# Kernel optimization log

Measured on AMD Instinct MI355X. Metric: run time of the kernel, lower is better.

## Reference

```python
import jax, jax.numpy as jnp
import numpy as np

H = 512       # hidden_dim == node_init_dim
N_MAX = 128   # max nodes (upper bound on ADD_NODE count)
L = 1024      # action sequence length (padded with -1)
NEG = -1e9    # mask value for invalid destination logits


def _gru(x, h, wih, whh, bih, bhh):
    # PyTorch nn.GRUCell math; gates packed as [r, z, n] along dim 0.
    gi = wih @ x + bih
    gh = whh @ h + bhh
    d = h.shape[0]
    r = jax.nn.sigmoid(gi[:d] + gh[:d])
    z = jax.nn.sigmoid(gi[d:2 * d] + gh[d:2 * d])
    n = jnp.tanh(gi[2 * d:] + r * gh[2 * d:])
    return (1.0 - z) * n + z * h


def _make_actions(rng):
    # Synthesize a grammatically valid DGMG teacher-forcing trace:
    # ADD_NODE=0, ADD_EDGE=1, CHOOSE_DEST=2, STOP_EDGE=3, STOP_NODE=4, pad=-1
    acts, ags = [], []
    cur = -1
    while len(acts) < L - 8 and cur < N_MAX - 1:
        acts.append(0); ags.append(0)
        cur += 1
        if cur > 0:
            for _ in range(int(rng.integers(1, 4))):
                if len(acts) >= L - 4:
                    break
                acts.append(1); ags.append(0)
                acts.append(2); ags.append(int(rng.integers(0, cur)))
            acts.append(3); ags.append(0)
    acts.append(4); ags.append(0)
    pad = L - len(acts)
    acts += [-1] * pad
    ags += [0] * pad
    return np.array(acts, np.int64), np.array(ags, np.int64)


def setup_inputs() -> dict:
    rng = np.random.default_rng(0)
    acts, ags = _make_actions(rng)
    key = jax.random.key(0)
    ks = jax.random.split(key, 12)
    s = 0.02
    p = lambda k, shape: jax.random.normal(k, shape, jnp.float32) * s
    return {
        "actions": jnp.asarray(acts),
        "args_seq": jnp.asarray(ags),
        "node_init": p(ks[0], (H,)),
        "w_nip": p(ks[1], (H, H)), "b_nip": jnp.zeros((H,), jnp.float32),
        "w_e1": p(ks[2], (H, 2 * H)), "b_e1": jnp.zeros((H,), jnp.float32),
        "w_e2": p(ks[3], (2, H)), "b_e2": jnp.zeros((2,), jnp.float32),
        "w_q": p(ks[4], (H, 2 * H)), "b_q": jnp.zeros((H,), jnp.float32),
        "w_k": p(ks[5], (H, H)), "b_k": jnp.zeros((H,), jnp.float32),
        "wih_n": p(ks[6], (3 * H, H)), "whh_n": p(ks[7], (3 * H, H)),
        "bih_n": jnp.zeros((3 * H,), jnp.float32), "bhh_n": jnp.zeros((3 * H,), jnp.float32),
        "wih_g": p(ks[8], (3 * H, H)), "whh_g": p(ks[9], (3 * H, H)),
        "bih_g": jnp.zeros((3 * H,), jnp.float32), "bhh_g": jnp.zeros((3 * H,), jnp.float32),
        "graph0": jnp.zeros((H,), jnp.float32),
    }


def reference(actions, args_seq, node_init, w_nip, b_nip, w_e1, b_e1, w_e2, b_e2,
              w_q, b_q, w_k, b_k, wih_n, whh_n, bih_n, bhh_n,
              wih_g, whh_g, bih_g, bhh_g, graph0):
    h0 = w_nip @ node_init + b_nip  # same fresh-node embedding for every ADD_NODE
    idx_range = jnp.arange(N_MAX)

    def edge_logits(g, curv):
        h = jax.nn.relu(w_e1 @ jnp.concatenate([g, curv]) + b_e1)
        return w_e2 @ h + b_e2  # (2,)

    def add_node(carry, arg):
        g, ne, cur, nll = carry
        cur2 = cur + 1
        ne2 = ne.at[cur2].set(h0)
        g2 = _gru(h0, g, wih_g, whh_g, bih_g, bhh_g)
        return (g2, ne2, cur2, nll)

    def add_edge(carry, arg):
        g, ne, cur, nll = carry
        nll2 = nll - jax.nn.log_softmax(edge_logits(g, ne[cur]))[0]
        return (g, ne, cur, nll2)

    def choose_dest(carry, arg):
        g, ne, cur, nll = carry
        curv = ne[cur]
        q = w_q @ jnp.concatenate([g, curv]) + b_q           # (H,)
        k = ne @ w_k.T + b_k                                  # (N_MAX, H)
        logits = jnp.where(idx_range < cur, k @ q, NEG)       # mask nodes >= cur
        nll2 = nll - jax.nn.log_softmax(logits)[arg]
        chosen = ne[arg]
        new_cur = _gru(chosen, curv, wih_n, whh_n, bih_n, bhh_n)
        ne2 = ne.at[cur].set(new_cur)
        g2 = _gru(new_cur, g, wih_g, whh_g, bih_g, bhh_g)
        return (g2, ne2, cur, nll2)

    def stop_edge(carry, arg):
        g, ne, cur, nll = carry
        nll2 = nll - jax.nn.log_softmax(edge_logits(g, ne[cur]))[1]
        return (g, ne, cur, nll2)

    def noop(carry, arg):
        return carry

    branches = [add_node, add_edge, choose_dest, stop_edge, noop]

    def step(carry, inp):
        a, arg = inp
        idx = jnp.where((a < 0) | (a >= 4), 4, a).astype(jnp.int32)
        return jax.lax.switch(idx, branches, carry, arg), None

    init = (graph0, jnp.zeros((N_MAX, H), graph0.dtype),
            jnp.int32(-1), jnp.zeros((), graph0.dtype))
    (g, ne, cur, nll), _ = jax.lax.scan(
        step, init, (actions.astype(jnp.int32), args_seq.astype(jnp.int32)))
    return nll
```

## Files before the change

kernel.cpp:

```cpp
#include <hip/hip_runtime.h>
#include <math.h>

#define NBLK 64
#define NTHR 576
#define LSEQ 1024

typedef unsigned int u32;
typedef unsigned short u16;
typedef unsigned long long u64;

__device__ __forceinline__ float bf2f(u16 u){ union{u32 i;float f;}v; v.i=(u32)u<<16; return v.f; }
__device__ __forceinline__ u16 f2bf(float f){ union{float f;u32 i;}v; v.f=f; u32 x=v.i;
  return (u16)((x + 0x7fffu + ((x>>16)&1u)) >> 16); }
__device__ __forceinline__ float u2f(u32 u){ union{u32 i;float f;}v; v.i=u; return v.f; }
__device__ __forceinline__ u32  f2u(float f){ union{float f;u32 i;}v; v.f=f; return v.i; }
__device__ __forceinline__ float sigm(float x){ return 1.f/(1.f+__expf(-x)); }

__device__ __forceinline__ u64 gld64(const u64* p){ return __hip_atomic_load(const_cast<u64*>(p), __ATOMIC_RELAXED, __HIP_MEMORY_SCOPE_AGENT); }
__device__ __forceinline__ void gst64(u64* p, u64 v){ __hip_atomic_store(p, v, __ATOMIC_RELAXED, __HIP_MEMORY_SCOPE_AGENT); }
__device__ __forceinline__ u64 pollt(const u64* p, u32 tag){
  u64 v; int n = 0;
  do { v = gld64(p); } while ((u32)(v>>32) != tag && ++n < (1<<20));
  return v;
}

__device__ __forceinline__ float wred(float a){
  a += __int_as_float(__builtin_amdgcn_update_dpp(0, __float_as_int(a), 0x111, 0xf, 0xf, true));
  a += __int_as_float(__builtin_amdgcn_update_dpp(0, __float_as_int(a), 0x112, 0xf, 0xf, true));
  a += __int_as_float(__builtin_amdgcn_update_dpp(0, __float_as_int(a), 0x114, 0xf, 0xf, true));
  a += __int_as_float(__builtin_amdgcn_update_dpp(0, __float_as_int(a), 0x118, 0xf, 0xf, true));
  a += __int_as_float(__builtin_amdgcn_update_dpp(0, __float_as_int(a), 0x142, 0xa, 0xf, true));
  a += __int_as_float(__builtin_amdgcn_update_dpp(0, __float_as_int(a), 0x143, 0xc, 0xf, true));
  return __int_as_float(__builtin_amdgcn_readlane(__float_as_int(a), 63));
}
__device__ __forceinline__ float wredsh(float a){
  #pragma unroll
  for (int off = 32; off; off >>= 1) a += __shfl_xor(a, off);
  return a;
}
__device__ __forceinline__ float wredmaxsh(float a){
  #pragma unroll
  for (int off = 32; off; off >>= 1) a = fmaxf(a, __shfl_xor(a, off));
  return a;
}

__device__ __forceinline__ float dot8p(uint4 w, float4 a, float4 b2){
  float s;
  s  = u2f(w.x<<16)*a.x  + u2f(w.x&0xffff0000u)*a.y;
  s += u2f(w.y<<16)*a.z  + u2f(w.y&0xffff0000u)*a.w;
  s += u2f(w.z<<16)*b2.x + u2f(w.z&0xffff0000u)*b2.y;
  s += u2f(w.w<<16)*b2.z + u2f(w.w&0xffff0000u)*b2.w;
  return s;
}
__device__ __forceinline__ float dot4f(float4 w, float4 x){
  return w.x*x.x + w.y*x.y + w.z*x.z + w.w*x.w;
}
__device__ __forceinline__ uint4 pk8(float4 a, float4 b2){
  uint4 r;
  r.x = (u32)f2bf(a.x)  | ((u32)f2bf(a.y)<<16);
  r.y = (u32)f2bf(a.z)  | ((u32)f2bf(a.w)<<16);
  r.z = (u32)f2bf(b2.x) | ((u32)f2bf(b2.y)<<16);
  r.w = (u32)f2bf(b2.z) | ((u32)f2bf(b2.w)<<16);
  return r;
}

#define SMEM_BYTES 150048

#define RUN_JOBS() do { \
  if (wv == 8){ \
    if (dBV && b == dBo1){ \
      u64 v_ = pollt(XS + dBSlot*64 + lane, dBTag); \
      float x0 = sA0 + bf2f((u16)(v_ & 0xffff)); \
      float x1 = sA1 + bf2f((u16)((v_>>16) & 0xffff)); \
      x0 = (lane < dBcur) ? x0 : -__builtin_inff(); \
      x1 = (lane + 64 < dBcur) ? x1 : -__builtin_inff(); \
      float m_ = wredmaxsh(fmaxf(x0, x1)); \
      float s_ = wredsh(__expf(x0 - m_) + __expf(x1 - m_)); \
      float la_ = (dBarg < 64) ? __shfl(x0, dBarg) : __shfl(x1, dBarg - 64); \
      if (lane == 0) nllw += (m_ + logf(s_)) - la_; \
    } \
    if (dAV && (b == dAo1 || b == dAo2)){ \
      const u64* P_ = XP + ((size_t)(dASlot*64 + lane))*64 + ((b == dAo2) ? 32 : 0); \
      float h0_ = 0.f, h1_ = 0.f; \
      for (int c_ = 0; c_ < 2; ++c_){ \
        u64 vv_[16]; int bad_; int nn_ = 0; \
        do { bad_ = 0; \
          _Pragma("unroll") for (int j_ = 0; j_ < 16; ++j_) vv_[j_] = gld64(P_ + c_*16 + j_); \
          _Pragma("unroll") for (int j_ = 0; j_ < 16; ++j_) bad_ |= ((u32)(vv_[j_]>>32) != dATag); \
        } while (bad_ && ++nn_ < (1<<20)); \
        _Pragma("unroll") for (int j_ = 0; j_ < 16; ++j_){ \
          h0_ += bf2f((u16)(vv_[j_] & 0xffff)); h1_ += bf2f((u16)((vv_[j_]>>16) & 0xffff)); } \
      } \
      if (b == dAo2) gst64(XS + dASlot*64 + lane, ((u64)dATag<<32) | (u32)f2bf(h0_) | ((u32)f2bf(h1_)<<16)); \
      else { sA0 = h0_; sA1 = h1_; } \
    } \
    if (aeV && b == aeOwn){ \
      u64 v_ = pollt(XE + aeSlot*64 + lane, aeTag); \
      float p0_ = wredsh(bf2f((u16)(v_ & 0xffff))); \
      float p1_ = wredsh(bf2f((u16)((v_>>16) & 0xffff))); \
      if (lane == 0){ \
        float l0_ = p0_ + be2_0, l1_ = p1_ + be2_1; \
        float m_ = fmaxf(l0_, l1_); \
        nllw += m_ + logf(__expf(l0_-m_) + __expf(l1_-m_)) - (aeSel ? l1_ : l0_); \
      } \
    } \
  } \
} while(0)

#define SHIFT_JOBS() do { \
  dBV = dAV; dBSlot = dASlot; dBo1 = dAo1; dBTag = dATag; dBcur = dAcur; dBarg = dAarg; \
  dAV = 0; aeV = 0; \
} while(0)

__global__ void __launch_bounds__(NTHR, 1)
dgmg_kernel(const int* __restrict__ actions, const int* __restrict__ argseq,
            const float* __restrict__ node_init, const float* __restrict__ w_nip, const float* __restrict__ b_nip,
            const float* __restrict__ w_e1, const float* __restrict__ b_e1,
            const float* __restrict__ w_e2, const float* __restrict__ b_e2,
            const float* __restrict__ w_q, const float* __restrict__ b_q,
            const float* __restrict__ w_k,
            const float* __restrict__ wih_n, const float* __restrict__ whh_n,
            const float* __restrict__ bih_n, const float* __restrict__ bhh_n,
            const float* __restrict__ wih_g, const float* __restrict__ whh_g,
            const float* __restrict__ bih_g, const float* __restrict__ bhh_g,
            const float* __restrict__ graph0,
            float* __restrict__ out, unsigned char* __restrict__ ws)
{
  extern __shared__ unsigned char smem[];
  u16* s_wihg = (u16*)smem;
  u16* s_whhg = s_wihg + 24*512;
  u16* s_wihn = s_whhg + 24*512;
  u16* s_whhn = s_wihn + 24*512;
  u16* s_we1  = s_whhn + 24*512;
  u16* s_wq   = s_we1 + 8*1024;
  float* s_g    = (float*)(s_wq + 8*1024);
  float* s_nc   = s_g + 512;
  float* s_curv = s_nc + 512;
  float* s_h0   = s_curv + 512;
  float* s_kloc = s_h0 + 512;
  float* s_bihg = s_kloc + 1024;
  float* s_bhhg = s_bihg + 24;
  float* s_bihn = s_bhhg + 24;
  float* s_bhhn = s_bihn + 24;
  float* s_be1  = s_bhhn + 24;
  float* s_bq   = s_be1 + 8;
  float* s_q8   = s_bq + 8;
  float* s_red  = s_q8 + 8;
  u16*   s_gin  = (u16*)(s_red + 16);

  const int b = blockIdx.x, tid = threadIdx.x;
  const int wv = tid >> 6, lane = tid & 63;
  const int d = b*8 + ((wv < 8) ? wv : 0);

  u64* Xng = (u64*)ws;
  u64* Xh  = Xng + 2048;
  u64* XE  = Xh + 512;
  u64* XP  = XE + 256;
  u64* XS  = XP + 16384;
  u64* XN  = XS + 256;

  if (tid < 24){
    int ld = tid/3, gt = tid%3;
    int row = gt*512 + b*8 + ld;
    s_bihg[tid] = bih_g[row]; s_bhhg[tid] = bhh_g[row];
    s_bihn[tid] = bih_n[row]; s_bhhn[tid] = bhh_n[row];
  }
  if (tid < 8){ s_be1[tid] = b_e1[b*8+tid]; s_bq[tid] = b_q[b*8+tid]; }

  for (int r = wv; r < 24; r += 9){
    int ld = r/3, gt = r%3;
    long grow = (long)(gt*512 + b*8 + ld) * 512;
    float4 a0, a1;
    a0 = *(const float4*)&wih_g[grow + lane*8]; a1 = *(const float4*)&wih_g[grow + lane*8 + 4];
    *(uint4*)&s_wihg[r*512 + lane*8] = pk8(a0, a1);
    a0 = *(const float4*)&whh_g[grow + lane*8]; a1 = *(const float4*)&whh_g[grow + lane*8 + 4];
    *(uint4*)&s_whhg[r*512 + lane*8] = pk8(a0, a1);
    a0 = *(const float4*)&wih_n[grow + lane*8]; a1 = *(const float4*)&wih_n[grow + lane*8 + 4];
    *(uint4*)&s_wihn[r*512 + lane*8] = pk8(a0, a1);
    a0 = *(const float4*)&whh_n[grow + lane*8]; a1 = *(const float4*)&whh_n[grow + lane*8 + 4];
    *(uint4*)&s_whhn[r*512 + lane*8] = pk8(a0, a1);
  }
  if (wv < 8){
    long grow = (long)(b*8 + wv) * 1024;
    #pragma unroll
    for (int h = 0; h < 2; ++h){
      float4 a0 = *(const float4*)&w_e1[grow + h*512 + lane*8];
      float4 a1 = *(const float4*)&w_e1[grow + h*512 + lane*8 + 4];
      *(uint4*)&s_we1[wv*1024 + h*512 + lane*8] = pk8(a0, a1);
      float4 q0 = *(const float4*)&w_q[grow + h*512 + lane*8];
      float4 q1 = *(const float4*)&w_q[grow + h*512 + lane*8 + 4];
      *(uint4*)&s_wq[wv*1024 + h*512 + lane*8] = pk8(q0, q1);
    }
  }
  float we2_0 = w_e2[d], we2_1 = w_e2[512+d];
  float be2_0 = b_e2[0], be2_1 = b_e2[1];
  float nllw = 0.f, sA0 = 0.f, sA1 = 0.f;

  int aeV=0, aeSlot=0, aeSel=0, aeOwn=0; u32 aeTag=0;
  int dAV=0, dASlot=0, dAo1=0, dAo2=0, dAcur=0, dAarg=0; u32 dATag=0;
  int dBV=0, dBSlot=0, dBo1=0, dBcur=0, dBarg=0; u32 dBTag=0;
  int ecnt=0, dcnt=0;

  if (tid < 512) s_g[tid] = node_init[tid];
  __syncthreads();
  float cbg_r=0,cbg_z=0,bg_ni=0,bg_nh=0, bh_gr=0,bh_gz=0;
  float bn_r=0,bn_z=0,bn_nh=0, fb_r=0,fb_z=0,fb_n=0, be1w=0,bqw=0;
  if (wv < 8){
    cbg_r = s_bihg[wv*3+0]+s_bhhg[wv*3+0];
    cbg_z = s_bihg[wv*3+1]+s_bhhg[wv*3+1];
    bg_ni = s_bihg[wv*3+2]; bg_nh = s_bhhg[wv*3+2];
    bh_gr = s_bhhg[wv*3+0]; bh_gz = s_bhhg[wv*3+1];
    bn_r = s_bhhn[wv*3+0]; bn_z = s_bhhn[wv*3+1]; bn_nh = s_bhhn[wv*3+2];
    fb_r = s_bihn[wv*3+0]; fb_z = s_bihn[wv*3+1]; fb_n = s_bihn[wv*3+2];
    be1w = s_be1[wv]; bqw = s_bq[wv];
    const float* wr = w_nip + (long)d*512;
    float4 wa = *(const float4*)&wr[lane*8], wb2 = *(const float4*)&wr[lane*8+4];
    float4 xa = *(float4*)&s_g[lane*8], xb = *(float4*)&s_g[lane*8+4];
    float h0d = wred(dot4f(wa,xa)+dot4f(wb2,xb)) + b_nip[d];
    if (lane == 0) gst64(&Xh[d], (1ull<<32) | f2u(h0d));
  }
  u32 ph = 2;

  float gi0r=0,gi0z=0,gi0n=0, ghn0r=0,ghn0z=0,ghn0n=0;
  int cur = -1, have_se = 0;
  bool first_an = true;

  for (int t = 0; t < LSEQ; ++t){
    int a = actions[t];
    if (a == 1) continue;
    if (a == 3){ have_se = 1; continue; }
    if (a < 0 || a >= 4) continue;

    int t1 = (t+1 < LSEQ) ? actions[t+1] : -1;
    int nxt = (t1 == 1);
    int i2 = (t+2 < LSEQ) ? t+2 : LSEQ-1;
    int chn = nxt ? argseq[i2] : 0;

    if (a == 0){
      int eslot = ecnt & 3;
      u32 tg = ph-1; int par = tg & 1;
      if (first_an){
        if (tid < 512){ u64 v = pollt(&Xh[tid], 1u); s_h0[tid] = u2f((u32)v); s_g[tid] = graph0[tid]; }
      } else {
        if (tid < 512){ u64 v = pollt(&Xng[(par*512+tid)*2+1], tg); s_g[tid] = u2f((u32)v); }
      }
      __syncthreads();
      RUN_JOBS();
      if (wv < 8){
        float4 xg_a = *(float4*)&s_g[lane*8], xg_b = *(float4*)&s_g[lane*8+4];
        float4 xc_a = *(float4*)&s_curv[lane*8], xc_b = *(float4*)&s_curv[lane*8+4];
        const u32* Whg = (const u32*)s_whhg;
        if (first_an){
          float4 xh_a = *(float4*)&s_h0[lane*8], xh_b = *(float4*)&s_h0[lane*8+4];
          const u32* Wig = (const u32*)s_wihg; const u32* Wn = (const u32*)s_whhn;
          gi0r = wred(dot8p(*(const uint4*)&Wig[(wv*3+0)*256+lane*4], xh_a,xh_b)) + s_bihg[wv*3+0];
          gi0z = wred(dot8p(*(const uint4*)&Wig[(wv*3+1)*256+lane*4], xh_a,xh_b)) + s_bihg[wv*3+1];
          gi0n = wred(dot8p(*(const uint4*)&Wig[(wv*3+2)*256+lane*4], xh_a,xh_b)) + s_bihg[wv*3+2];
          ghn0r = wred(dot8p(*(const uint4*)&Wn[(wv*3+0)*256+lane*4], xh_a,xh_b)) + bn_r;
          ghn0z = wred(dot8p(*(const uint4*)&Wn[(wv*3+1)*256+lane*4], xh_a,xh_b)) + bn_z;
          ghn0n = wred(dot8p(*(const uint4*)&Wn[(wv*3+2)*256+lane*4], xh_a,xh_b)) + bn_nh;
        }
        {
          float ghr = wred(dot8p(*(const uint4*)&Whg[(wv*3+0)*256+lane*4], xg_a,xg_b)) + bh_gr;
          float ghz = wred(dot8p(*(const uint4*)&Whg[(wv*3+1)*256+lane*4], xg_a,xg_b)) + bh_gz;
          float ghn = wred(dot8p(*(const uint4*)&Whg[(wv*3+2)*256+lane*4], xg_a,xg_b)) + bg_nh;
          float r_ = sigm(gi0r + ghr), z_ = sigm(gi0z + ghz);
          float n_ = tanhf(gi0n + r_*ghn);
          if (lane == 0) gst64(&Xng[((ph&1)*512+d)*2+1], ((u64)ph<<32) | f2u((1.f-z_)*n_ + z_*s_g[d]));
        }
        if (nxt){
          float gr = bf2f(s_gin[chn*24+wv*3+0]), gz = bf2f(s_gin[chn*24+wv*3+1]), gn = bf2f(s_gin[chn*24+wv*3+2]);
          float r2 = sigm(gr + ghn0r), z2 = sigm(gz + ghn0z);
          float n2 = tanhf(gn + r2*ghn0n);
          if (lane == 0) gst64(&Xng[((ph&1)*512+d)*2], ((u64)ph<<32) | f2u((1.f-z2)*n2 + z2*s_h0[d]));
        }
        if (cur >= 0){
          const u32* Win = (const u32*)s_wihn;
          float fr = wred(dot8p(*(const uint4*)&Win[(wv*3+0)*256+lane*4], xc_a,xc_b)) + fb_r;
          float fz = wred(dot8p(*(const uint4*)&Win[(wv*3+1)*256+lane*4], xc_a,xc_b)) + fb_z;
          float fn = wred(dot8p(*(const uint4*)&Win[(wv*3+2)*256+lane*4], xc_a,xc_b)) + fb_n;
          const float* wkr = w_k + (long)d*512;
          float4 ka = *(const float4*)&wkr[lane*8], kb2 = *(const float4*)&wkr[lane*8+4];
          float kv = wred(dot4f(ka,xc_a)+dot4f(kb2,xc_b));
          if (lane == 0){
            s_gin[cur*24+wv*3+0] = f2bf(fr); s_gin[cur*24+wv*3+1] = f2bf(fz); s_gin[cur*24+wv*3+2] = f2bf(fn);
            s_kloc[wv*128 + cur] = kv;
          }
        }
        if (have_se){
          const u32* Re = (const u32*)s_we1 + wv*512;
          float pe = dot8p(*(const uint4*)&Re[lane*4], xg_a,xg_b) + dot8p(*(const uint4*)&Re[256+lane*4], xc_a,xc_b);
          float hv = fmaxf(wred(pe) + be1w, 0.f);
          if (lane == 0){ s_red[wv*2] = hv*we2_0; s_red[wv*2+1] = hv*we2_1; }
        }
      }
      __syncthreads();
      if (have_se && tid == 0){
        float p0 = 0.f, p1 = 0.f;
        #pragma unroll
        for (int i = 0; i < 8; ++i){ p0 += s_red[i*2]; p1 += s_red[i*2+1]; }
        gst64(&XE[eslot*64 + b], ((u64)ph<<32) | (u32)f2bf(p0) | ((u32)f2bf(p1)<<16));
      }
      if (tid < 512) s_curv[tid] = s_h0[tid];
      SHIFT_JOBS();
      if (have_se){ aeV=1; aeSlot=eslot; aeSel=1; aeOwn=ecnt&63; aeTag=ph; ecnt++; }
      have_se = 0; first_an = false;
      cur += 1; ph += 1;
    }
    else {
      int arg = argseq[t];
      int eslot = ecnt & 3, dslot = dcnt & 3;
      u32 tg = ph-1; int par = tg & 1;
      if (tid < 512){
        u64 v0, v1; int n = 0;
        const u64* p = &Xng[(par*512 + tid)*2];
        do { v0 = gld64(p); v1 = gld64(p+1); }
        while ((((u32)(v0>>32) != tg) || ((u32)(v1>>32) != tg)) && ++n < (1<<20));
        s_nc[tid] = u2f((u32)v0); s_g[tid] = u2f((u32)v1);
      }
      __syncthreads();
      RUN_JOBS();
      if (wv < 8){
        float4 xn_a = *(float4*)&s_nc[lane*8], xn_b = *(float4*)&s_nc[lane*8+4];
        float4 xg_a = *(float4*)&s_g[lane*8],  xg_b = *(float4*)&s_g[lane*8+4];
        float4 xc_a = *(float4*)&s_curv[lane*8], xc_b = *(float4*)&s_curv[lane*8+4];
        const u32* Wn = (const u32*)s_whhn; const u32* Wig = (const u32*)s_wihg; const u32* Whg = (const u32*)s_whhg;
        if (nxt){
          float ghr = wred(dot8p(*(const uint4*)&Wn[(wv*3+0)*256+lane*4], xn_a,xn_b)) + bn_r;
          float ghz = wred(dot8p(*(const uint4*)&Wn[(wv*3+1)*256+lane*4], xn_a,xn_b)) + bn_z;
          float ghn = wred(dot8p(*(const uint4*)&Wn[(wv*3+2)*256+lane*4], xn_a,xn_b)) + bn_nh;
          float gr = bf2f(s_gin[chn*24+wv*3+0]), gz = bf2f(s_gin[chn*24+wv*3+1]), gn = bf2f(s_gin[chn*24+wv*3+2]);
          float r_ = sigm(gr+ghr), z_ = sigm(gz+ghz);
          float n_ = tanhf(gn + r_*ghn);
          if (lane == 0) gst64(&Xng[((ph&1)*512+d)*2], ((u64)ph<<32) | f2u((1.f-z_)*n_ + z_*s_nc[d]));
        }
        {
          float pr = dot8p(*(const uint4*)&Wig[(wv*3+0)*256+lane*4], xn_a,xn_b)
                   + dot8p(*(const uint4*)&Whg[(wv*3+0)*256+lane*4], xg_a,xg_b);
          float pz = dot8p(*(const uint4*)&Wig[(wv*3+1)*256+lane*4], xn_a,xn_b)
                   + dot8p(*(const uint4*)&Whg[(wv*3+1)*256+lane*4], xg_a,xg_b);
          float r_ = sigm(wred(pr) + cbg_r);
          float z_ = sigm(wred(pz) + cbg_z);
          float gin_ = wred(dot8p(*(const uint4*)&Wig[(wv*3+2)*256+lane*4], xn_a,xn_b)) + bg_ni;
          float ghn_ = wred(dot8p(*(const uint4*)&Whg[(wv*3+2)*256+lane*4], xg_a,xg_b)) + bg_nh;
          float n_ = tanhf(gin_ + r_*ghn_);
          if (lane == 0) gst64(&Xng[((ph&1)*512+d)*2+1], ((u64)ph<<32) | f2u((1.f-z_)*n_ + z_*s_g[d]));
        }
        {
          const u32* Rq = (const u32*)s_wq + wv*512;
          float pq = dot8p(*(const uint4*)&Rq[lane*4], xg_a,xg_b) + dot8p(*(const uint4*)&Rq[256+lane*4], xc_a,xc_b);
          float qd = wred(pq) + bqw;
          const u32* Re = (const u32*)s_we1 + wv*512;
          float pe = dot8p(*(const uint4*)&Re[lane*4], xg_a,xg_b) + dot8p(*(const uint4*)&Re[256+lane*4], xc_a,xc_b);
          float hv = fmaxf(wred(pe) + be1w, 0.f);
          if (lane == 0){ s_q8[wv] = qd; s_red[wv*2] = hv*we2_0; s_red[wv*2+1] = hv*we2_1; }
        }
      }
      __syncthreads();
      if (tid < 64){
        float pl0 = 0.f, pl1 = 0.f;
        #pragma unroll
        for (int k = 0; k < 8; ++k){
          pl0 += s_kloc[k*128 + tid]      * s_q8[k];
          pl1 += s_kloc[k*128 + tid + 64] * s_q8[k];
        }
        gst64(&XP[((size_t)(dslot*64 + tid))*64 + b], ((u64)ph<<32) | (u32)f2bf(pl0) | ((u32)f2bf(pl1)<<16));
      }
      if (tid == 64){
        float p0 = 0.f, p1 = 0.f;
        #pragma unroll
        for (int i = 0; i < 8; ++i){ p0 += s_red[i*2]; p1 += s_red[i*2+1]; }
        gst64(&XE[eslot*64 + b], ((u64)ph<<32) | (u32)f2bf(p0) | ((u32)f2bf(p1)<<16));
      }
      if (tid < 512) s_curv[tid] = s_nc[tid];
      SHIFT_JOBS();
      aeV=1; aeSlot=eslot; aeSel=0; aeOwn=ecnt&63; aeTag=ph; ecnt++;
      dAV=1; dASlot=dslot; dAo1=(2*dcnt)&63; dAo2=(2*dcnt+1)&63; dAcur=cur; dAarg=arg; dATag=ph;
      dcnt++;
      ph += 1;
    }
  }

  {
    int eslot = ecnt & 3;
    u32 tg = ph-1; int par = tg & 1;
    if (tid < 512){ u64 v = pollt(&Xng[(par*512+tid)*2+1], tg); s_g[tid] = u2f((u32)v); }
    __syncthreads();
    RUN_JOBS();
    if (have_se && wv < 8){
      float4 xg_a = *(float4*)&s_g[lane*8], xg_b = *(float4*)&s_g[lane*8+4];
      float4 xc_a = *(float4*)&s_curv[lane*8], xc_b = *(float4*)&s_curv[lane*8+4];
      const u32* Re = (const u32*)s_we1 + wv*512;
      float pe = dot8p(*(const uint4*)&Re[lane*4], xg_a,xg_b) + dot8p(*(const uint4*)&Re[256+lane*4], xc_a,xc_b);
      float hv = fmaxf(wred(pe) + be1w, 0.f);
      if (lane == 0){ s_red[wv*2] = hv*we2_0; s_red[wv*2+1] = hv*we2_1; }
    }
    __syncthreads();
    if (have_se && tid == 0){
      float p0 = 0.f, p1 = 0.f;
      #pragma unroll
      for (int i = 0; i < 8; ++i){ p0 += s_red[i*2]; p1 += s_red[i*2+1]; }
      gst64(&XE[eslot*64 + b], ((u64)ph<<32) | (u32)f2bf(p0) | ((u32)f2bf(p1)<<16));
    }
    SHIFT_JOBS();
    RUN_JOBS();
    if (wv == 8){
      if (have_se && b == 0){
        u64 v = pollt(&XE[eslot*64 + lane], ph);
        float p0 = wredsh(bf2f((u16)(v & 0xffff)));
        float p1 = wredsh(bf2f((u16)((v>>16) & 0xffff)));
        if (lane == 0){
          float l0 = p0 + be2_0, l1 = p1 + be2_1;
          float m = fmaxf(l0, l1);
          nllw += m + logf(__expf(l0-m) + __expf(l1-m)) - l1;
        }
      }
      if (lane == 0) gst64(&XN[b], (0xFFFFull<<32) | f2u(nllw));
      if (b == 0){
        u64 v = pollt(&XN[lane], 0xFFFFu);
        float tot = wredsh(u2f((u32)v));
        if (lane == 0) out[0] = tot;
      }
    }
  }
}

extern "C" void kernel_launch(void* const* d_in, const int* in_sizes, int n_in,
                              void* d_out, int out_size, void* d_ws, size_t ws_size,
                              hipStream_t stream) {
  (void)in_sizes; (void)n_in; (void)out_size; (void)ws_size;
  hipMemsetAsync(d_ws, 0, 156160, stream);
  hipFuncSetAttribute((const void*)dgmg_kernel,
                      hipFuncAttributeMaxDynamicSharedMemorySize, SMEM_BYTES);
  dgmg_kernel<<<NBLK, NTHR, SMEM_BYTES, stream>>>(
      (const int*)d_in[0], (const int*)d_in[1],
      (const float*)d_in[2], (const float*)d_in[3], (const float*)d_in[4],
      (const float*)d_in[5], (const float*)d_in[6],
      (const float*)d_in[7], (const float*)d_in[8],
      (const float*)d_in[9], (const float*)d_in[10],
      (const float*)d_in[11],
      (const float*)d_in[13], (const float*)d_in[14],
      (const float*)d_in[15], (const float*)d_in[16],
      (const float*)d_in[17], (const float*)d_in[18],
      (const float*)d_in[19], (const float*)d_in[20],
      (const float*)d_in[21],
      (float*)d_out, (unsigned char*)d_ws);
}
```

Before: 1.102 ms.

## Remove second per-step block barrier by double-buffering and deferring publish to wave 8

Shared-memory vectors (s_g, s_nc, s_curv, s_q8, s_red) become parity-indexed double buffers. This lets the end-of-step __syncthreads and the thread-0/tid<64 publish of the edge and dest partial sums be removed; those reductions are now done by wave 8 at the start of the next step, with the job pipeline deepened by one stage and two drain iterations added at the end. It also reuses the freshly computed node input gates when the next chosen node is the current one, and reorders the GRU computations. The cost is a longer cross-block dependency chain, more shared memory and more complex state shifting, which could add latency to the polling chain.

```diff
diff --git a/kernel.cpp b/kernel.cpp
--- a/kernel.cpp
+++ b/kernel.cpp
@@ -64,52 +64,69 @@
   return r;
 }
 
-#define SMEM_BYTES 150048
-
-#define RUN_JOBS() do { \
+#define SMEM_BYTES 156288
+
+#define W8_FIRE_AND_JOBS() do { \
   if (wv == 8){ \
-    if (dBV && b == dBo1){ \
-      u64 v_ = pollt(XS + dBSlot*64 + lane, dBTag); \
+    int par1_ = (int)((ph-1)&1); \
+    if (d0V){ \
+      float pl0 = 0.f, pl1 = 0.f; \
+      _Pragma("unroll") for (int k = 0; k < 8; ++k){ \
+        float qk = s_q8[par1_*8 + k]; \
+        pl0 += s_kloc[k*128 + lane]      * qk; \
+        pl1 += s_kloc[k*128 + lane + 64] * qk; } \
+      gst64(&XP[((size_t)(d0Slot*64 + lane))*64 + b], ((u64)d0Tag<<32) | (u32)f2bf(pl0) | ((u32)f2bf(pl1)<<16)); \
+    } \
+    if (e0V && lane == 0){ \
+      float p0 = 0.f, p1 = 0.f; \
+      _Pragma("unroll") for (int i = 0; i < 8; ++i){ p0 += s_red[par1_*16 + i*2]; p1 += s_red[par1_*16 + i*2+1]; } \
+      gst64(&XE[e0Slot*64 + b], ((u64)e0Tag<<32) | (u32)f2bf(p0) | ((u32)f2bf(p1)<<16)); \
+    } \
+    if (d2V && b == d2o1){  \
+      u64 v_ = pollt(XS + d2Slot*64 + lane, d2Tag); \
       float x0 = sA0 + bf2f((u16)(v_ & 0xffff)); \
       float x1 = sA1 + bf2f((u16)((v_>>16) & 0xffff)); \
-      x0 = (lane < dBcur) ? x0 : -__builtin_inff(); \
-      x1 = (lane + 64 < dBcur) ? x1 : -__builtin_inff(); \
+      x0 = (lane < d2cur)      ? x0 : -__builtin_inff(); \
+      x1 = (lane + 64 < d2cur) ? x1 : -__builtin_inff(); \
       float m_ = wredmaxsh(fmaxf(x0, x1)); \
       float s_ = wredsh(__expf(x0 - m_) + __expf(x1 - m_)); \
-      float la_ = (dBarg < 64) ? __shfl(x0, dBarg) : __shfl(x1, dBarg - 64); \
+      float la_ = (d2arg < 64) ? __shfl(x0, d2arg) : __shfl(x1, d2arg - 64); \
       if (lane == 0) nllw += (m_ + logf(s_)) - la_; \
     } \
-    if (dAV && (b == dAo1 || b == dAo2)){ \
-      const u64* P_ = XP + ((size_t)(dASlot*64 + lane))*64 + ((b == dAo2) ? 32 : 0); \
+    if (d1V && (b == d1o1 || b == d1o2)){  \
+      const u64* P_ = XP + ((size_t)(d1Slot*64 + lane))*64 + ((b == d1o2) ? 32 : 0); \
       float h0_ = 0.f, h1_ = 0.f; \
       for (int c_ = 0; c_ < 2; ++c_){ \
         u64 vv_[16]; int bad_; int nn_ = 0; \
         do { bad_ = 0; \
           _Pragma("unroll") for (int j_ = 0; j_ < 16; ++j_) vv_[j_] = gld64(P_ + c_*16 + j_); \
-          _Pragma("unroll") for (int j_ = 0; j_ < 16; ++j_) bad_ |= ((u32)(vv_[j_]>>32) != dATag); \
+          _Pragma("unroll") for (int j_ = 0; j_ < 16; ++j_) bad_ |= ((u32)(vv_[j_]>>32) != d1Tag); \
         } while (bad_ && ++nn_ < (1<<20)); \
         _Pragma("unroll") for (int j_ = 0; j_ < 16; ++j_){ \
           h0_ += bf2f((u16)(vv_[j_] & 0xffff)); h1_ += bf2f((u16)((vv_[j_]>>16) & 0xffff)); } \
       } \
-      if (b == dAo2) gst64(XS + dASlot*64 + lane, ((u64)dATag<<32) | (u32)f2bf(h0_) | ((u32)f2bf(h1_)<<16)); \
+      if (b == d1o2) gst64(XS + d1Slot*64 + lane, ((u64)d1Tag<<32) | (u32)f2bf(h0_) | ((u32)f2bf(h1_)<<16)); \
       else { sA0 = h0_; sA1 = h1_; } \
     } \
-    if (aeV && b == aeOwn){ \
-      u64 v_ = pollt(XE + aeSlot*64 + lane, aeTag); \
+    if (e1V && b == e1Own){  \
+      u64 v_ = pollt(XE + e1Slot*64 + lane, e1Tag); \
       float p0_ = wredsh(bf2f((u16)(v_ & 0xffff))); \
       float p1_ = wredsh(bf2f((u16)((v_>>16) & 0xffff))); \
       if (lane == 0){ \
         float l0_ = p0_ + be2_0, l1_ = p1_ + be2_1; \
         float m_ = fmaxf(l0_, l1_); \
-        nllw += m_ + logf(__expf(l0_-m_) + __expf(l1_-m_)) - (aeSel ? l1_ : l0_); \
+        nllw += m_ + logf(__expf(l0_-m_) + __expf(l1_-m_)) - (e1Sel ? l1_ : l0_); \
       } \
     } \
   } \
 } while(0)
 
-#define SHIFT_JOBS() do { \
-  dBV = dAV; dBSlot = dASlot; dBo1 = dAo1; dBTag = dATag; dBcur = dAcur; dBarg = dAarg; \
-  dAV = 0; aeV = 0; \
+#define SHIFT2() do { \
+  d2V=d1V; d2Slot=d1Slot; d2o1=d1o1; d2Tag=d1Tag; d2cur=d1cur; d2arg=d1arg; \
+  d1V=d0V; d1Slot=d0Slot; d1o1=d0o1; d1o2=d0o2; d1Tag=d0Tag; d1cur=d0cur; d1arg=d0arg; \
+  d0V=0; \
+  e1V=e0V; e1Slot=e0Slot; e1Own=e0Own; e1Tag=e0Tag; e1Sel=e0Sel; \
+  e0V=0; \
 } while(0)
 
 __global__ void __launch_bounds__(NTHR, 1)
@@ -134,9 +151,9 @@
   u16* s_we1  = s_whhn + 24*512;
   u16* s_wq   = s_we1 + 8*1024;
   float* s_g    = (float*)(s_wq + 8*1024);
-  float* s_nc   = s_g + 512;
-  float* s_curv = s_nc + 512;
-  float* s_h0   = s_curv + 512;
+  float* s_nc   = s_g + 1024;
+  float* s_curv = s_nc + 1024;
+  float* s_h0   = s_curv + 1024;
   float* s_kloc = s_h0 + 512;
   float* s_bihg = s_kloc + 1024;
   float* s_bhhg = s_bihg + 24;
@@ -145,8 +162,8 @@
   float* s_be1  = s_bhhn + 24;
   float* s_bq   = s_be1 + 8;
   float* s_q8   = s_bq + 8;
-  float* s_red  = s_q8 + 8;
-  u16*   s_gin  = (u16*)(s_red + 16);
+  float* s_red  = s_q8 + 16;
+  u16*   s_gin  = (u16*)(s_red + 32);
 
   const int b = blockIdx.x, tid = threadIdx.x;
   const int wv = tid >> 6, lane = tid & 63;
@@ -196,9 +213,11 @@
   float be2_0 = b_e2[0], be2_1 = b_e2[1];
   float nllw = 0.f, sA0 = 0.f, sA1 = 0.f;
 
-  int aeV=0, aeSlot=0, aeSel=0, aeOwn=0; u32 aeTag=0;
-  int dAV=0, dASlot=0, dAo1=0, dAo2=0, dAcur=0, dAarg=0; u32 dATag=0;
-  int dBV=0, dBSlot=0, dBo1=0, dBcur=0, dBarg=0; u32 dBTag=0;
+  int d0V=0,d0Slot=0,d0o1=0,d0o2=0,d0cur=0,d0arg=0; u32 d0Tag=0;
+  int d1V=0,d1Slot=0,d1o1=0,d1o2=0,d1cur=0,d1arg=0; u32 d1Tag=0;
+  int d2V=0,d2Slot=0,d2o1=0,d2cur=0,d2arg=0; u32 d2Tag=0;
+  int e0V=0,e0Slot=0,e0Own=0,e0Sel=0; u32 e0Tag=0;
+  int e1V=0,e1Slot=0,e1Own=0,e1Sel=0; u32 e1Tag=0;
   int ecnt=0, dcnt=0;
 
   if (tid < 512) s_g[tid] = node_init[tid];
@@ -219,6 +238,7 @@
     float h0d = wred(dot4f(wa,xa)+dot4f(wb2,xb)) + b_nip[d];
     if (lane == 0) gst64(&Xh[d], (1ull<<32) | f2u(h0d));
   }
+  __syncthreads();
   u32 ph = 2;
 
   float gi0r=0,gi0z=0,gi0n=0, ghn0r=0,ghn0z=0,ghn0n=0;
@@ -236,19 +256,19 @@
     int i2 = (t+2 < LSEQ) ? t+2 : LSEQ-1;
     int chn = nxt ? argseq[i2] : 0;
 
+    u32 tg = ph-1; int par1 = tg & 1, par = ph & 1;
+
     if (a == 0){
-      int eslot = ecnt & 3;
-      u32 tg = ph-1; int par = tg & 1;
       if (first_an){
-        if (tid < 512){ u64 v = pollt(&Xh[tid], 1u); s_h0[tid] = u2f((u32)v); s_g[tid] = graph0[tid]; }
+        if (tid < 512){ u64 v = pollt(&Xh[tid], 1u); s_h0[tid] = u2f((u32)v); s_g[par1*512+tid] = graph0[tid]; }
       } else {
-        if (tid < 512){ u64 v = pollt(&Xng[(par*512+tid)*2+1], tg); s_g[tid] = u2f((u32)v); }
+        if (tid < 512){ u64 v = pollt(&Xng[(par1*512+tid)*2+1], tg); s_g[par1*512+tid] = u2f((u32)v); }
       }
       __syncthreads();
-      RUN_JOBS();
+      W8_FIRE_AND_JOBS();
       if (wv < 8){
-        float4 xg_a = *(float4*)&s_g[lane*8], xg_b = *(float4*)&s_g[lane*8+4];
-        float4 xc_a = *(float4*)&s_curv[lane*8], xc_b = *(float4*)&s_curv[lane*8+4];
+        float4 xg_a = *(float4*)&s_g[par1*512+lane*8], xg_b = *(float4*)&s_g[par1*512+lane*8+4];
+        float4 xc_a = *(float4*)&s_curv[par1*512+lane*8], xc_b = *(float4*)&s_curv[par1*512+lane*8+4];
         const u32* Whg = (const u32*)s_whhg;
         if (first_an){
           float4 xh_a = *(float4*)&s_h0[lane*8], xh_b = *(float4*)&s_h0[lane*8+4];
@@ -266,19 +286,14 @@
           float ghn = wred(dot8p(*(const uint4*)&Whg[(wv*3+2)*256+lane*4], xg_a,xg_b)) + bg_nh;
           float r_ = sigm(gi0r + ghr), z_ = sigm(gi0z + ghz);
           float n_ = tanhf(gi0n + r_*ghn);
-          if (lane == 0) gst64(&Xng[((ph&1)*512+d)*2+1], ((u64)ph<<32) | f2u((1.f-z_)*n_ + z_*s_g[d]));
-        }
-        if (nxt){
-          float gr = bf2f(s_gin[chn*24+wv*3+0]), gz = bf2f(s_gin[chn*24+wv*3+1]), gn = bf2f(s_gin[chn*24+wv*3+2]);
-          float r2 = sigm(gr + ghn0r), z2 = sigm(gz + ghn0z);
-          float n2 = tanhf(gn + r2*ghn0n);
-          if (lane == 0) gst64(&Xng[((ph&1)*512+d)*2], ((u64)ph<<32) | f2u((1.f-z2)*n2 + z2*s_h0[d]));
-        }
+          if (lane == 0) gst64(&Xng[((ph&1)*512+d)*2+1], ((u64)ph<<32) | f2u((1.f-z_)*n_ + z_*s_g[par1*512+d]));
+        }
+        float fr=0.f, fz=0.f, fn=0.f;
         if (cur >= 0){
           const u32* Win = (const u32*)s_wihn;
-          float fr = wred(dot8p(*(const uint4*)&Win[(wv*3+0)*256+lane*4], xc_a,xc_b)) + fb_r;
-          float fz = wred(dot8p(*(const uint4*)&Win[(wv*3+1)*256+lane*4], xc_a,xc_b)) + fb_z;
-          float fn = wred(dot8p(*(const uint4*)&Win[(wv*3+2)*256+lane*4], xc_a,xc_b)) + fb_n;
+          fr = wred(dot8p(*(const uint4*)&Win[(wv*3+0)*256+lane*4], xc_a,xc_b)) + fb_r;
+          fz = wred(dot8p(*(const uint4*)&Win[(wv*3+1)*256+lane*4], xc_a,xc_b)) + fb_z;
+          fn = wred(dot8p(*(const uint4*)&Win[(wv*3+2)*256+lane*4], xc_a,xc_b)) + fb_n;
           const float* wkr = w_k + (long)d*512;
           float4 ka = *(const float4*)&wkr[lane*8], kb2 = *(const float4*)&wkr[lane*8+4];
           float kv = wred(dot4f(ka,xc_a)+dot4f(kb2,xc_b));
@@ -287,53 +302,43 @@
             s_kloc[wv*128 + cur] = kv;
           }
         }
+        if (nxt){
+          float gr = (chn == cur) ? fr : bf2f(s_gin[chn*24+wv*3+0]);
+          float gz = (chn == cur) ? fz : bf2f(s_gin[chn*24+wv*3+1]);
+          float gn = (chn == cur) ? fn : bf2f(s_gin[chn*24+wv*3+2]);
+          float r2 = sigm(gr + ghn0r), z2 = sigm(gz + ghn0z);
+          float n2 = tanhf(gn + r2*ghn0n);
+          if (lane == 0) gst64(&Xng[((ph&1)*512+d)*2], ((u64)ph<<32) | f2u((1.f-z2)*n2 + z2*s_h0[d]));
+        }
         if (have_se){
           const u32* Re = (const u32*)s_we1 + wv*512;
           float pe = dot8p(*(const uint4*)&Re[lane*4], xg_a,xg_b) + dot8p(*(const uint4*)&Re[256+lane*4], xc_a,xc_b);
           float hv = fmaxf(wred(pe) + be1w, 0.f);
-          if (lane == 0){ s_red[wv*2] = hv*we2_0; s_red[wv*2+1] = hv*we2_1; }
+          if (lane == 0){ s_red[par*16 + wv*2] = hv*we2_0; s_red[par*16 + wv*2+1] = hv*we2_1; }
         }
       }
-      __syncthreads();
-      if (have_se && tid == 0){
-        float p0 = 0.f, p1 = 0.f;
-        #pragma unroll
-        for (int i = 0; i < 8; ++i){ p0 += s_red[i*2]; p1 += s_red[i*2+1]; }
-        gst64(&XE[eslot*64 + b], ((u64)ph<<32) | (u32)f2bf(p0) | ((u32)f2bf(p1)<<16));
-      }
-      if (tid < 512) s_curv[tid] = s_h0[tid];
-      SHIFT_JOBS();
-      if (have_se){ aeV=1; aeSlot=eslot; aeSel=1; aeOwn=ecnt&63; aeTag=ph; ecnt++; }
+      if (tid < 512) s_curv[par*512+tid] = s_h0[tid];
+      SHIFT2();
+      if (have_se){ e0V=1; e0Slot=ecnt&3; e0Sel=1; e0Own=ecnt&63; e0Tag=ph; ecnt++; }
       have_se = 0; first_an = false;
       cur += 1; ph += 1;
     }
     else {
       int arg = argseq[t];
-      int eslot = ecnt & 3, dslot = dcnt & 3;
-      u32 tg = ph-1; int par = tg & 1;
       if (tid < 512){
+        const u64* p = &Xng[(par1*512 + tid)*2];
         u64 v0, v1; int n = 0;
-        const u64* p = &Xng[(par*512 + tid)*2];
         do { v0 = gld64(p); v1 = gld64(p+1); }
         while ((((u32)(v0>>32) != tg) || ((u32)(v1>>32) != tg)) && ++n < (1<<20));
-        s_nc[tid] = u2f((u32)v0); s_g[tid] = u2f((u32)v1);
+        s_nc[par1*512+tid] = u2f((u32)v0); s_g[par1*512+tid] = u2f((u32)v1);
       }
       __syncthreads();
-      RUN_JOBS();
+      W8_FIRE_AND_JOBS();
       if (wv < 8){
-        float4 xn_a = *(float4*)&s_nc[lane*8], xn_b = *(float4*)&s_nc[lane*8+4];
-        float4 xg_a = *(float4*)&s_g[lane*8],  xg_b = *(float4*)&s_g[lane*8+4];
-        float4 xc_a = *(float4*)&s_curv[lane*8], xc_b = *(float4*)&s_curv[lane*8+4];
+        float4 xn_a = *(float4*)&s_nc[par1*512+lane*8], xn_b = *(float4*)&s_nc[par1*512+lane*8+4];
+        float4 xg_a = *(float4*)&s_g[par1*512+lane*8],  xg_b = *(float4*)&s_g[par1*512+lane*8+4];
+        float4 xc_a = *(float4*)&s_curv[par1*512+lane*8], xc_b = *(float4*)&s_curv[par1*512+lane*8+4];
         const u32* Wn = (const u32*)s_whhn; const u32* Wig = (const u32*)s_wihg; const u32* Whg = (const u32*)s_whhg;
-        if (nxt){
-          float ghr = wred(dot8p(*(const uint4*)&Wn[(wv*3+0)*256+lane*4], xn_a,xn_b)) + bn_r;
-          float ghz = wred(dot8p(*(const uint4*)&Wn[(wv*3+1)*256+lane*4], xn_a,xn_b)) + bn_z;
-          float ghn = wred(dot8p(*(const uint4*)&Wn[(wv*3+2)*256+lane*4], xn_a,xn_b)) + bn_nh;
-          float gr = bf2f(s_gin[chn*24+wv*3+0]), gz = bf2f(s_gin[chn*24+wv*3+1]), gn = bf2f(s_gin[chn*24+wv*3+2]);
-          float r_ = sigm(gr+ghr), z_ = sigm(gz+ghz);
-          float n_ = tanhf(gn + r_*ghn);
-          if (lane == 0) gst64(&Xng[((ph&1)*512+d)*2], ((u64)ph<<32) | f2u((1.f-z_)*n_ + z_*s_nc[d]));
-        }
         {
           float pr = dot8p(*(const uint4*)&Wig[(wv*3+0)*256+lane*4], xn_a,xn_b)
                    + dot8p(*(const uint4*)&Whg[(wv*3+0)*256+lane*4], xg_a,xg_b);
@@ -344,7 +349,16 @@
           float gin_ = wred(dot8p(*(const uint4*)&Wig[(wv*3+2)*256+lane*4], xn_a,xn_b)) + bg_ni;
           float ghn_ = wred(dot8p(*(const uint4*)&Whg[(wv*3+2)*256+lane*4], xg_a,xg_b)) + bg_nh;
           float n_ = tanhf(gin_ + r_*ghn_);
-          if (lane == 0) gst64(&Xng[((ph&1)*512+d)*2+1], ((u64)ph<<32) | f2u((1.f-z_)*n_ + z_*s_g[d]));
+          if (lane == 0) gst64(&Xng[((ph&1)*512+d)*2+1], ((u64)ph<<32) | f2u((1.f-z_)*n_ + z_*s_g[par1*512+d]));
+        }
+        if (nxt){
+          float ghr = wred(dot8p(*(const uint4*)&Wn[(wv*3+0)*256+lane*4], xn_a,xn_b)) + bn_r;
+          float ghz = wred(dot8p(*(const uint4*)&Wn[(wv*3+1)*256+lane*4], xn_a,xn_b)) + bn_z;
+          float ghn = wred(dot8p(*(const uint4*)&Wn[(wv*3+2)*256+lane*4], xn_a,xn_b)) + bn_nh;
+          float gr = bf2f(s_gin[chn*24+wv*3+0]), gz = bf2f(s_gin[chn*24+wv*3+1]), gn = bf2f(s_gin[chn*24+wv*3+2]);
+          float r_ = sigm(gr+ghr), z_ = sigm(gz+ghz);
+          float n_ = tanhf(gn + r_*ghn);
+          if (lane == 0) gst64(&Xng[((ph&1)*512+d)*2], ((u64)ph<<32) | f2u((1.f-z_)*n_ + z_*s_nc[par1*512+d]));
         }
         {
           const u32* Rq = (const u32*)s_wq + wv*512;
@@ -353,74 +367,47 @@
           const u32* Re = (const u32*)s_we1 + wv*512;
           float pe = dot8p(*(const uint4*)&Re[lane*4], xg_a,xg_b) + dot8p(*(const uint4*)&Re[256+lane*4], xc_a,xc_b);
           float hv = fmaxf(wred(pe) + be1w, 0.f);
-          if (lane == 0){ s_q8[wv] = qd; s_red[wv*2] = hv*we2_0; s_red[wv*2+1] = hv*we2_1; }
+          if (lane == 0){ s_q8[par*8+wv] = qd; s_red[par*16+wv*2] = hv*we2_0; s_red[par*16+wv*2+1] = hv*we2_1; }
         }
       }
-      __syncthreads();
-      if (tid < 64){
-        float pl0 = 0.f, pl1 = 0.f;
-        #pragma unroll
-        for (int k = 0; k < 8; ++k){
-          pl0 += s_kloc[k*128 + tid]      * s_q8[k];
-          pl1 += s_kloc[k*128 + tid + 64] * s_q8[k];
-        }
-        gst64(&XP[((size_t)(dslot*64 + tid))*64 + b], ((u64)ph<<32) | (u32)f2bf(pl0) | ((u32)f2bf(pl1)<<16));
-      }
-      if (tid == 64){
-        float p0 = 0.f, p1 = 0.f;
-        #pragma unroll
-        for (int i = 0; i < 8; ++i){ p0 += s_red[i*2]; p1 += s_red[i*2+1]; }
-        gst64(&XE[eslot*64 + b], ((u64)ph<<32) | (u32)f2bf(p0) | ((u32)f2bf(p1)<<16));
-      }
-      if (tid < 512) s_curv[tid] = s_nc[tid];
-      SHIFT_JOBS();
-      aeV=1; aeSlot=eslot; aeSel=0; aeOwn=ecnt&63; aeTag=ph; ecnt++;
-      dAV=1; dASlot=dslot; dAo1=(2*dcnt)&63; dAo2=(2*dcnt+1)&63; dAcur=cur; dAarg=arg; dATag=ph;
-      dcnt++;
+      if (tid < 512) s_curv[par*512+tid] = s_nc[par1*512+tid];
+      SHIFT2();
+      e0V=1; e0Slot=ecnt&3; e0Sel=0; e0Own=ecnt&63; e0Tag=ph; ecnt++;
+      d0V=1; d0Slot=dcnt&3; d0o1=(2*dcnt)&63; d0o2=(2*dcnt+1)&63; d0cur=cur; d0arg=arg; d0Tag=ph; dcnt++;
       ph += 1;
     }
   }
 
   {
-    int eslot = ecnt & 3;
-    u32 tg = ph-1; int par = tg & 1;
-    if (tid < 512){ u64 v = pollt(&Xng[(par*512+tid)*2+1], tg); s_g[tid] = u2f((u32)v); }
+    u32 tg = ph-1; int par1 = tg & 1, par = ph & 1;
+    if (tid < 512){ u64 v = pollt(&Xng[(par1*512+tid)*2+1], tg); s_g[par1*512+tid] = u2f((u32)v); }
     __syncthreads();
-    RUN_JOBS();
+    W8_FIRE_AND_JOBS();
     if (have_se && wv < 8){
-      float4 xg_a = *(float4*)&s_g[lane*8], xg_b = *(float4*)&s_g[lane*8+4];
-      float4 xc_a = *(float4*)&s_curv[lane*8], xc_b = *(float4*)&s_curv[lane*8+4];
+      float4 xg_a = *(float4*)&s_g[par1*512+lane*8], xg_b = *(float4*)&s_g[par1*512+lane*8+4];
+      float4 xc_a = *(float4*)&s_curv[par1*512+lane*8], xc_b = *(float4*)&s_curv[par1*512+lane*8+4];
       const u32* Re = (const u32*)s_we1 + wv*512;
       float pe = dot8p(*(const uint4*)&Re[lane*4], xg_a,xg_b) + dot8p(*(const uint4*)&Re[256+lane*4], xc_a,xc_b);
       float hv = fmaxf(wred(pe) + be1w, 0.f);
-      if (lane == 0){ s_red[wv*2] = hv*we2_0; s_red[wv*2+1] = hv*we2_1; }
+      if (lane == 0){ s_red[par*16+wv*2] = hv*we2_0; s_red[par*16+wv*2+1] = hv*we2_1; }
     }
+    SHIFT2();
+    if (have_se){ e0V=1; e0Slot=ecnt&3; e0Sel=1; e0Own=ecnt&63; e0Tag=ph; ecnt++; }
+    ph += 1;
+  }
+  #pragma unroll 1
+  for (int dp = 0; dp < 2; ++dp){
     __syncthreads();
-    if (have_se && tid == 0){
-      float p0 = 0.f, p1 = 0.f;
-      #pragma unroll
-      for (int i = 0; i < 8; ++i){ p0 += s_red[i*2]; p1 += s_red[i*2+1]; }
-      gst64(&XE[eslot*64 + b], ((u64)ph<<32) | (u32)f2bf(p0) | ((u32)f2bf(p1)<<16));
-    }
-    SHIFT_JOBS();
-    RUN_JOBS();
-    if (wv == 8){
-      if (have_se && b == 0){
-        u64 v = pollt(&XE[eslot*64 + lane], ph);
-        float p0 = wredsh(bf2f((u16)(v & 0xffff)));
-        float p1 = wredsh(bf2f((u16)((v>>16) & 0xffff)));
-        if (lane == 0){
-          float l0 = p0 + be2_0, l1 = p1 + be2_1;
-          float m = fmaxf(l0, l1);
-          nllw += m + logf(__expf(l0-m) + __expf(l1-m)) - l1;
-        }
-      }
-      if (lane == 0) gst64(&XN[b], (0xFFFFull<<32) | f2u(nllw));
-      if (b == 0){
-        u64 v = pollt(&XN[lane], 0xFFFFu);
-        float tot = wredsh(u2f((u32)v));
-        if (lane == 0) out[0] = tot;
-      }
+    W8_FIRE_AND_JOBS();
+    SHIFT2();
+    ph += 1;
+  }
+  if (wv == 8){
+    if (lane == 0) gst64(&XN[b], (0xFFFFull<<32) | f2u(nllw));
+    if (b == 0){
+      u64 v = pollt(&XN[lane], 0xFFFFu);
+      float tot = wredsh(u2f((u32)v));
+      if (lane == 0) out[0] = tot;
     }
   }
 }
```

Result: slower. 1.269 ms (+15.2%).
